# Kernel tuning notes

Hardware: AMD Instinct MI355X
Metric: run time of the kernel (lower is better)

The kernel has to match this reference:

```python
import jax, jax.numpy as jnp
import numpy as np

EMB_DIM = 256
NUM_HEADS = 4
HEAD_DIM = EMB_DIM // NUM_HEADS
N_EDGES = 320000
N_NODES = 10000
EPS = 1e-16  # torch_geometric softmax epsilon


def setup_inputs() -> dict:
    key = jax.random.key(0)
    kq, kk, ki, kw1, kb1, kw2 = jax.random.split(key, 6)
    q = jax.random.normal(kq, (N_EDGES, EMB_DIM), dtype=jnp.float32)
    k = jax.random.normal(kk, (N_EDGES, EMB_DIM), dtype=jnp.float32)
    index = jnp.sort(jax.random.randint(ki, (N_EDGES,), 0, N_NODES, dtype=jnp.int32))
    # xavier_uniform with gain 1/sqrt(2)
    lim1 = (1.0 / np.sqrt(2.0)) * np.sqrt(6.0 / (2 * EMB_DIM + EMB_DIM))
    w1_w = jax.random.uniform(kw1, (EMB_DIM, 2 * EMB_DIM), dtype=jnp.float32, minval=-lim1, maxval=lim1)
    w1_b = jnp.zeros((EMB_DIM,), dtype=jnp.float32)
    lim2 = (1.0 / np.sqrt(2.0)) * np.sqrt(6.0 / (NUM_HEADS + HEAD_DIM))
    w2 = jax.random.uniform(kw2, (NUM_HEADS, HEAD_DIM), dtype=jnp.float32, minval=-lim2, maxval=lim2)
    return {"q": q, "k": k, "w1_w": w1_w, "w1_b": w1_b, "w2": w2,
            "index": index, "dim_size": N_NODES}


def _segment_softmax(src, index, num_segments):
    # src: [E, H, 1]; index: [E] segment ids; stable softmax per segment per head
    seg_max = jax.ops.segment_max(src, index, num_segments=num_segments)  # [N, H, 1]
    out = jnp.exp(src - seg_max[index])
    seg_sum = jax.ops.segment_sum(out, index, num_segments=num_segments)  # [N, H, 1]
    return out / (seg_sum[index] + EPS)


def reference(q, k, w1_w, w1_b, w2, index, dim_size):
    x = jnp.concatenate([q, k], axis=1)                      # [E, 2D]
    x = x @ w1_w.T + w1_b                                    # [E, D]
    x = jax.nn.leaky_relu(x, negative_slope=0.01)
    x = x.reshape(-1, NUM_HEADS, HEAD_DIM)                   # [E, H, C]
    attn = jnp.einsum('nhc,hc->nh', x, w2)[..., None]        # [E, H, 1]
    return _segment_softmax(attn, index, dim_size)
```

## Files before the change

kernel.cpp:

```cpp
#include <hip/hip_runtime.h>
#include <hip/hip_bf16.h>


typedef __attribute__((ext_vector_type(8))) short bf16x8;
typedef __attribute__((ext_vector_type(4))) float f32x4;

#define NNODES 10000

__device__ __forceinline__ short f2bf(float f) {
    __hip_bfloat16 h = __float2bfloat16(f);
    return *reinterpret_cast<short*>(&h);
}

__global__ __launch_bounds__(512) void attn_gemm(
    const float* __restrict__ q, const float* __restrict__ kk_,
    const float* __restrict__ w1, const float* __restrict__ b1,
    const float* __restrict__ w2, float* __restrict__ attn, int nE)
{
    __shared__ short lds_a[128 * 64];
    __shared__ short lds_b[256 * 64];

    const int tid  = threadIdx.x;
    const int lane = tid & 63;
    const int w    = tid >> 6;
    const int wm   = w >> 1;
    const int wn   = w & 1;
    const int l15  = lane & 15;
    const int lhi  = lane >> 4;
    const int row0 = blockIdx.x * 128;

    f32x4 acc[2][8];
#pragma unroll
    for (int i = 0; i < 2; ++i)
#pragma unroll
        for (int j = 0; j < 8; ++j) acc[i][j] = (f32x4){0.f, 0.f, 0.f, 0.f};

    for (int kt = 0; kt < 8; ++kt) {
        const int k0 = kt * 64;
#pragma unroll
        for (int it = 0; it < 2; ++it) {
            int slot = it * 512 + tid;
            int m = slot >> 3, k8 = slot & 7;
            int j = k0 + k8 * 8;
            const float* src = (j < 256) ? (q + (size_t)(row0 + m) * 256 + j)
                                         : (kk_ + (size_t)(row0 + m) * 256 + (j - 256));
            float4 v0 = *(const float4*)src;
            float4 v1 = *(const float4*)(src + 4);
            bf16x8 pk;
            pk[0] = f2bf(v0.x); pk[1] = f2bf(v0.y); pk[2] = f2bf(v0.z); pk[3] = f2bf(v0.w);
            pk[4] = f2bf(v1.x); pk[5] = f2bf(v1.y); pk[6] = f2bf(v1.z); pk[7] = f2bf(v1.w);
            int idx = (m * 64 + k8 * 8) ^ ((m & 7) << 3);
            *(bf16x8*)(lds_a + idx) = pk;
        }
#pragma unroll
        for (int it = 0; it < 4; ++it) {
            int slot = it * 512 + tid;
            int d = slot >> 3, k8 = slot & 7;
            const float* src = w1 + (size_t)d * 512 + k0 + k8 * 8;
            float4 v0 = *(const float4*)src;
            float4 v1 = *(const float4*)(src + 4);
            bf16x8 pk;
            pk[0] = f2bf(v0.x); pk[1] = f2bf(v0.y); pk[2] = f2bf(v0.z); pk[3] = f2bf(v0.w);
            pk[4] = f2bf(v1.x); pk[5] = f2bf(v1.y); pk[6] = f2bf(v1.z); pk[7] = f2bf(v1.w);
            int idx = (d * 64 + k8 * 8) ^ ((d & 7) << 3);
            *(bf16x8*)(lds_b + idx) = pk;
        }
        __syncthreads();

#pragma unroll
        for (int ks = 0; ks < 2; ++ks) {
            const int kkq = ks * 32 + lhi * 8;
            bf16x8 af[2], bfv[8];
#pragma unroll
            for (int fm = 0; fm < 2; ++fm) {
                int r = wm * 32 + fm * 16 + l15;
                af[fm] = *(const bf16x8*)(lds_a + ((r * 64 + kkq) ^ ((r & 7) << 3)));
            }
#pragma unroll
            for (int fn = 0; fn < 8; ++fn) {
                int c = wn * 128 + fn * 16 + l15;
                bfv[fn] = *(const bf16x8*)(lds_b + ((c * 64 + kkq) ^ ((c & 7) << 3)));
            }
#pragma unroll
            for (int fm = 0; fm < 2; ++fm)
#pragma unroll
                for (int fn = 0; fn < 8; ++fn)
                    acc[fm][fn] = __builtin_amdgcn_mfma_f32_16x16x32_bf16(
                        af[fm], bfv[fn], acc[fm][fn], 0, 0, 0);
        }
        __syncthreads();
    }

    float bias[8], w2v[8];
#pragma unroll
    for (int fn = 0; fn < 8; ++fn) {
        int col = wn * 128 + fn * 16 + l15;
        bias[fn] = b1[col];
        w2v[fn]  = w2[col];
    }
#pragma unroll
    for (int fm = 0; fm < 2; ++fm) {
#pragma unroll
        for (int r = 0; r < 4; ++r) {
            int row = row0 + wm * 32 + fm * 16 + lhi * 4 + r;
            float p0 = 0.f, p1 = 0.f;
#pragma unroll
            for (int fn = 0; fn < 4; ++fn) {
                float y = acc[fm][fn][r] + bias[fn];
                y = (y > 0.f) ? y : 0.01f * y;
                p0 += y * w2v[fn];
            }
#pragma unroll
            for (int fn = 4; fn < 8; ++fn) {
                float y = acc[fm][fn][r] + bias[fn];
                y = (y > 0.f) ? y : 0.01f * y;
                p1 += y * w2v[fn];
            }
#pragma unroll
            for (int m = 1; m < 16; m <<= 1) {
                p0 += __shfl_xor(p0, m);
                p1 += __shfl_xor(p1, m);
            }
            if (l15 == 0) {
                attn[(size_t)row * 4 + wn * 2 + 0] = p0;
                attn[(size_t)row * 4 + wn * 2 + 1] = p1;
            }
        }
    }
}

__device__ __forceinline__ unsigned fenc(float f) {
    unsigned u = __float_as_uint(f);
    return (u & 0x80000000u) ? ~u : (u | 0x80000000u);
}
__device__ __forceinline__ float fdec(unsigned k) {
    return (k & 0x80000000u) ? __uint_as_float(k ^ 0x80000000u) : __uint_as_float(~k);
}

__global__ void seg_init(unsigned* __restrict__ segmax, float* __restrict__ segsum, int n) {
    int i = blockIdx.x * blockDim.x + threadIdx.x;
    if (i < n) { segmax[i] = 0u; segsum[i] = 0.f; }
}

__global__ void seg_max(const float* __restrict__ attn, const int* __restrict__ index,
                        unsigned* __restrict__ segmax, int total) {
    int i = blockIdx.x * blockDim.x + threadIdx.x;
    if (i >= total) return;
    int e = i >> 2, h = i & 3;
    atomicMax(&segmax[index[e] * 4 + h], fenc(attn[i]));
}

__global__ void seg_expsum(float* __restrict__ attn, const int* __restrict__ index,
                           const unsigned* __restrict__ segmax, float* __restrict__ segsum,
                           int total) {
    int i = blockIdx.x * blockDim.x + threadIdx.x;
    if (i >= total) return;
    int e = i >> 2, h = i & 3;
    float m = fdec(segmax[index[e] * 4 + h]);
    float ex = expf(attn[i] - m);
    attn[i] = ex;
    atomicAdd(&segsum[index[e] * 4 + h], ex);
}

__global__ void seg_norm(const float* __restrict__ attn, const int* __restrict__ index,
                         const float* __restrict__ segsum, float* __restrict__ out, int total) {
    int i = blockIdx.x * blockDim.x + threadIdx.x;
    if (i >= total) return;
    int e = i >> 2, h = i & 3;
    out[i] = attn[i] / (segsum[index[e] * 4 + h] + 1e-16f);
}

extern "C" void kernel_launch(void* const* d_in, const int* in_sizes, int n_in,
                              void* d_out, int out_size, void* d_ws, size_t ws_size,
                              hipStream_t stream) {
    const float* q   = (const float*)d_in[0];
    const float* k   = (const float*)d_in[1];
    const float* w1  = (const float*)d_in[2];
    const float* b1  = (const float*)d_in[3];
    const float* w2  = (const float*)d_in[4];
    const int* index = (const int*)d_in[5];

    const int nE = in_sizes[0] / 256;
    float*    attn   = (float*)d_ws;
    unsigned* segmax = (unsigned*)((char*)d_ws + (size_t)nE * 4 * 4);
    float*    segsum = (float*)((char*)segmax + (size_t)NNODES * 4 * 4);
    float*    out    = (float*)d_out;

    attn_gemm<<<nE / 128, 512, 0, stream>>>(q, k, w1, b1, w2, attn, nE);

    int nseg = NNODES * 4;
    seg_init<<<(nseg + 255) / 256, 256, 0, stream>>>(segmax, segsum, nseg);

    int total = nE * 4;
    int blks = (total + 255) / 256;
    seg_max<<<blks, 256, 0, stream>>>(attn, index, segmax, total);
    seg_expsum<<<blks, 256, 0, stream>>>(attn, index, segmax, segsum, total);
    seg_norm<<<blks, 256, 0, stream>>>(attn, index, segsum, out, total);
}
```

Baseline: 268.5 us.

## Double-buffer GEMM tiles via direct global-to-LDS loads with pre-converted bf16 weights

Adds a small kernel that converts W1 to bf16 once per call, and rewrites the GEMM main loop to stream fp32 activations and bf16 weights straight into LDS with global_load_lds. The LDS buffers are double-buffered so the next K-slice loads while MFMAs run on the current one. Activations are converted to bf16 when read from LDS, and the K-step shrinks to 32 with one barrier per step. The trade-offs are double the LDS footprint (fp32 A tiles), extra conversion work in the inner loop, and an extra kernel launch.

```diff
diff --git a/kernel.cpp b/kernel.cpp
--- a/kernel.cpp
+++ b/kernel.cpp
@@ -4,6 +4,7 @@
 
 typedef __attribute__((ext_vector_type(8))) short bf16x8;
 typedef __attribute__((ext_vector_type(4))) float f32x4;
+typedef __attribute__((ext_vector_type(4))) short s16x4;
 
 #define NNODES 10000
 
@@ -12,13 +13,26 @@
     return *reinterpret_cast<short*>(&h);
 }
 
-__global__ __launch_bounds__(512) void attn_gemm(
+__device__ __forceinline__ void gload_lds16(const void* g, void* l) {
+    __builtin_amdgcn_global_load_lds(
+        (const __attribute__((address_space(1))) unsigned int*)g,
+        (__attribute__((address_space(3))) unsigned int*)l, 16, 0, 0);
+}
+
+__global__ void w1_cvt(const float* __restrict__ w1, short* __restrict__ w1b) {
+    int i = (blockIdx.x * 256 + threadIdx.x) * 4;
+    float4 v = *(const float4*)(w1 + i);
+    s16x4 o; o[0] = f2bf(v.x); o[1] = f2bf(v.y); o[2] = f2bf(v.z); o[3] = f2bf(v.w);
+    *(s16x4*)(w1b + i) = o;
+}
+
+__global__ __launch_bounds__(512, 4) void attn_gemm(
     const float* __restrict__ q, const float* __restrict__ kk_,
-    const float* __restrict__ w1, const float* __restrict__ b1,
-    const float* __restrict__ w2, float* __restrict__ attn, int nE)
+    const short* __restrict__ w1b, const float* __restrict__ b1,
+    const float* __restrict__ w2, float* __restrict__ attn)
 {
-    __shared__ short lds_a[128 * 64];
-    __shared__ short lds_b[256 * 64];
+    __shared__ float lds_a[2][4096];
+    __shared__ short lds_b[2][8192];
 
     const int tid  = threadIdx.x;
     const int lane = tid & 63;
@@ -29,67 +43,68 @@
     const int lhi  = lane >> 4;
     const int row0 = blockIdx.x * 128;
 
+    const int a_row  = w * 8 + (lane >> 3);
+    const int a_csrc = (lane & 7) ^ (lane >> 3);
+    const int b_d    = w * 16 + (lane >> 2);
+    const int b_csrc = (lane & 3) ^ ((lane >> 3) & 3);
+
     f32x4 acc[2][8];
 #pragma unroll
     for (int i = 0; i < 2; ++i)
 #pragma unroll
         for (int j = 0; j < 8; ++j) acc[i][j] = (f32x4){0.f, 0.f, 0.f, 0.f};
 
-    for (int kt = 0; kt < 8; ++kt) {
-        const int k0 = kt * 64;
-#pragma unroll
-        for (int it = 0; it < 2; ++it) {
-            int slot = it * 512 + tid;
-            int m = slot >> 3, k8 = slot & 7;
-            int j = k0 + k8 * 8;
-            const float* src = (j < 256) ? (q + (size_t)(row0 + m) * 256 + j)
-                                         : (kk_ + (size_t)(row0 + m) * 256 + (j - 256));
-            float4 v0 = *(const float4*)src;
-            float4 v1 = *(const float4*)(src + 4);
+    size_t a_off[2], b_off[2];
+#pragma unroll
+    for (int i = 0; i < 2; ++i) {
+        a_off[i] = (size_t)(row0 + i * 64 + a_row) * 256 + a_csrc * 4;
+        b_off[i] = (size_t)(i * 128 + b_d) * 512 + b_csrc * 8;
+    }
+
+#define STAGE(buf, kt)                                                          \
+    {                                                                           \
+        const float* abase = ((kt) < 8) ? q : kk_;                              \
+        const int koff = ((kt) & 7) * 32;                                       \
+        gload_lds16(abase + a_off[0] + koff,                                    \
+                    (char*)&lds_a[buf][0] + (0 * 8 + w) * 1024);                \
+        gload_lds16(abase + a_off[1] + koff,                                    \
+                    (char*)&lds_a[buf][0] + (1 * 8 + w) * 1024);                \
+        gload_lds16(w1b + b_off[0] + (kt) * 32,                                 \
+                    (char*)&lds_b[buf][0] + (0 * 8 + w) * 1024);                \
+        gload_lds16(w1b + b_off[1] + (kt) * 32,                                 \
+                    (char*)&lds_b[buf][0] + (1 * 8 + w) * 1024);                \
+    }
+
+    STAGE(0, 0);
+    __syncthreads();
+
+#pragma unroll
+    for (int kt = 0; kt < 16; ++kt) {
+        const int cur = kt & 1;
+        if (kt < 15) STAGE(cur ^ 1, kt + 1);
+
+        bf16x8 af[2];
+#pragma unroll
+        for (int fm = 0; fm < 2; ++fm) {
+            const int r = wm * 32 + fm * 16 + l15;
+            const float* As = &lds_a[cur][r * 32];
+            f32x4 a0 = *(const f32x4*)(As + (((2 * lhi)     ^ (r & 7)) * 4));
+            f32x4 a1 = *(const f32x4*)(As + (((2 * lhi + 1) ^ (r & 7)) * 4));
             bf16x8 pk;
-            pk[0] = f2bf(v0.x); pk[1] = f2bf(v0.y); pk[2] = f2bf(v0.z); pk[3] = f2bf(v0.w);
-            pk[4] = f2bf(v1.x); pk[5] = f2bf(v1.y); pk[6] = f2bf(v1.z); pk[7] = f2bf(v1.w);
-            int idx = (m * 64 + k8 * 8) ^ ((m & 7) << 3);
-            *(bf16x8*)(lds_a + idx) = pk;
+            pk[0] = f2bf(a0[0]); pk[1] = f2bf(a0[1]); pk[2] = f2bf(a0[2]); pk[3] = f2bf(a0[3]);
+            pk[4] = f2bf(a1[0]); pk[5] = f2bf(a1[1]); pk[6] = f2bf(a1[2]); pk[7] = f2bf(a1[3]);
+            af[fm] = pk;
         }
 #pragma unroll
-        for (int it = 0; it < 4; ++it) {
-            int slot = it * 512 + tid;
-            int d = slot >> 3, k8 = slot & 7;
-            const float* src = w1 + (size_t)d * 512 + k0 + k8 * 8;
-            float4 v0 = *(const float4*)src;
-            float4 v1 = *(const float4*)(src + 4);
-            bf16x8 pk;
-            pk[0] = f2bf(v0.x); pk[1] = f2bf(v0.y); pk[2] = f2bf(v0.z); pk[3] = f2bf(v0.w);
-            pk[4] = f2bf(v1.x); pk[5] = f2bf(v1.y); pk[6] = f2bf(v1.z); pk[7] = f2bf(v1.w);
-            int idx = (d * 64 + k8 * 8) ^ ((d & 7) << 3);
-            *(bf16x8*)(lds_b + idx) = pk;
+        for (int fn = 0; fn < 8; ++fn) {
+            const int d = wn * 128 + fn * 16 + l15;
+            bf16x8 bfv = *(const bf16x8*)(&lds_b[cur][d * 32 + ((lhi ^ ((d >> 1) & 3)) * 8)]);
+            acc[0][fn] = __builtin_amdgcn_mfma_f32_16x16x32_bf16(af[0], bfv, acc[0][fn], 0, 0, 0);
+            acc[1][fn] = __builtin_amdgcn_mfma_f32_16x16x32_bf16(af[1], bfv, acc[1][fn], 0, 0, 0);
         }
         __syncthreads();
-
-#pragma unroll
-        for (int ks = 0; ks < 2; ++ks) {
-            const int kkq = ks * 32 + lhi * 8;
-            bf16x8 af[2], bfv[8];
-#pragma unroll
-            for (int fm = 0; fm < 2; ++fm) {
-                int r = wm * 32 + fm * 16 + l15;
-                af[fm] = *(const bf16x8*)(lds_a + ((r * 64 + kkq) ^ ((r & 7) << 3)));
-            }
-#pragma unroll
-            for (int fn = 0; fn < 8; ++fn) {
-                int c = wn * 128 + fn * 16 + l15;
-                bfv[fn] = *(const bf16x8*)(lds_b + ((c * 64 + kkq) ^ ((c & 7) << 3)));
-            }
-#pragma unroll
-            for (int fm = 0; fm < 2; ++fm)
-#pragma unroll
-                for (int fn = 0; fn < 8; ++fn)
-                    acc[fm][fn] = __builtin_amdgcn_mfma_f32_16x16x32_bf16(
-                        af[fm], bfv[fn], acc[fm][fn], 0, 0, 0);
-        }
-        __syncthreads();
-    }
+    }
+#undef STAGE
 
     float bias[8], w2v[8];
 #pragma unroll
@@ -181,15 +196,19 @@
     const int* index = (const int*)d_in[5];
 
     const int nE = in_sizes[0] / 256;
-    float*    attn   = (float*)d_ws;
-    unsigned* segmax = (unsigned*)((char*)d_ws + (size_t)nE * 4 * 4);
-    float*    segsum = (float*)((char*)segmax + (size_t)NNODES * 4 * 4);
+    char* ws = (char*)d_ws;
+    float*    attn   = (float*)ws;                       ws += (size_t)nE * 4 * 4;
+    unsigned* segmax = (unsigned*)ws;                    ws += (size_t)NNODES * 4 * 4;
+    float*    segsum = (float*)ws;                       ws += (size_t)NNODES * 4 * 4;
+    short*    w1bf   = (short*)ws;
     float*    out    = (float*)d_out;
 
-    attn_gemm<<<nE / 128, 512, 0, stream>>>(q, k, w1, b1, w2, attn, nE);
+    w1_cvt<<<128, 256, 0, stream>>>(w1, w1bf);
 
     int nseg = NNODES * 4;
     seg_init<<<(nseg + 255) / 256, 256, 0, stream>>>(segmax, segsum, nseg);
+
+    attn_gemm<<<nE / 128, 512, 0, stream>>>(q, k, w1bf, b1, w2, attn);
 
     int total = nE * 4;
     int blks = (total + 255) / 256;
```

Result: faster. 220.1 us (-18.0%).
